# Performance work log

Measured on AMD Instinct MI355X. Metric: run time of the kernel, lower is better.

The kernel has to match this reference:

```python
import jax, jax.numpy as jnp
import numpy as np
from jax.ops import segment_sum

N_NODES = 50000
N_EDGES = 800000
NUM_FEAT = 16
EDGE_DIM = 8
H = 100
L = 2
BN_EPS = 1e-5


def setup_inputs() -> dict:
    key = jax.random.key(0)
    ks = iter(jax.random.split(key, 40))
    def w(shape, scale=0.05):
        return (jax.random.normal(next(ks), shape, dtype=jnp.float32) * scale)
    inp = {
        "x": jax.random.normal(next(ks), (N_NODES, NUM_FEAT), dtype=jnp.float32),
        "edge_index": jax.random.randint(next(ks), (2, N_EDGES), 0, N_NODES, dtype=jnp.int64) if jax.config.jax_enable_x64 else jax.random.randint(next(ks), (2, N_EDGES), 0, N_NODES).astype(jnp.int32),
        "edge_attr": jax.random.normal(next(ks), (N_EDGES, EDGE_DIM), dtype=jnp.float32),
        # embeddings
        "node_w": w((NUM_FEAT, H)), "node_b": w((H,)),
        "edge_w": w((EDGE_DIM, H)), "edge_b": w((H,)),
        # per-layer GINEConv MLP (stacked over layers)
        "conv_w1": w((L, H, H)), "conv_b1": w((L, H)),
        "conv_w2": w((L, H, H)), "conv_b2": w((L, H)),
        # batchnorm affine params
        "bn_gamma": jnp.ones((L, H), dtype=jnp.float32), "bn_beta": jnp.zeros((L, H), dtype=jnp.float32),
        # per-layer edge-update MLP
        "emlp_w1": w((L, 3 * H, H)), "emlp_b1": w((L, H)),
        "emlp_w2": w((L, H, H)), "emlp_b2": w((L, H)),
        # final classifier MLP (3H -> 50 -> 25 -> 2); dropout is identity at eval
        "mlp_w1": w((3 * H, 50)), "mlp_b1": w((50,)),
        "mlp_w2": w((50, 25)), "mlp_b2": w((25,)),
        "mlp_w3": w((25, 2)), "mlp_b3": w((2,)),
    }
    return inp


def reference(x, edge_index, edge_attr,
              node_w, node_b, edge_w, edge_b,
              conv_w1, conv_b1, conv_w2, conv_b2,
              bn_gamma, bn_beta,
              emlp_w1, emlp_b1, emlp_w2, emlp_b2,
              mlp_w1, mlp_b1, mlp_w2, mlp_b2, mlp_w3, mlp_b3):
    src, dst = edge_index[0], edge_index[1]
    n_nodes = x.shape[0]

    h = x @ node_w + node_b          # [N, H]
    e = edge_attr @ edge_w + edge_b  # [E, H]

    for i in range(L):
        # GINEConv: out_i = nn((1+eps)*h_i + sum_{e: dst=i} relu(h_src + e)); eps=0
        msg = jax.nn.relu(h[src] + e)                       # [E, H] gather + combine
        agg = segment_sum(msg, dst, num_segments=n_nodes)   # [N, H] scatter-add
        z = h + agg
        z = jax.nn.relu(z @ conv_w1[i] + conv_b1[i]) @ conv_w2[i] + conv_b2[i]
        # BatchNorm (train mode: batch stats over nodes, biased variance)
        mu = jnp.mean(z, axis=0)
        var = jnp.var(z, axis=0)
        z = (z - mu) * jax.lax.rsqrt(var + BN_EPS) * bn_gamma[i] + bn_beta[i]
        h = (h + jax.nn.relu(z)) * 0.5
        # edge update: e += MLP([h_src, h_dst, e]) / 2
        cat = jnp.concatenate([h[src], h[dst], e], axis=-1)  # [E, 3H]
        upd = jax.nn.relu(cat @ emlp_w1[i] + emlp_b1[i]) @ emlp_w2[i] + emlp_b2[i]
        e = e + upd * 0.5

    # per-edge features: relu([h_src, h_dst]) ++ e  -> [E, 3H]
    feat = jnp.concatenate([jax.nn.relu(jnp.concatenate([h[src], h[dst]], axis=-1)), e], axis=-1)
    out = jax.nn.relu(feat @ mlp_w1 + mlp_b1)
    out = jax.nn.relu(out @ mlp_w2 + mlp_b2)
    return out @ mlp_w3 + mlp_b3  # [E, 2]
```

## Files before the change

### kernel.cpp

```cpp
#include <hip/hip_runtime.h>
#include <hip/hip_bf16.h>

#define N_NODES 50000
#define N_EDGES 800000
#define HDIM 100
#define ESTR 104

typedef _Float16 half8_t __attribute__((ext_vector_type(8)));
typedef _Float16 half4_t __attribute__((ext_vector_type(4)));
typedef float f32x4_t __attribute__((ext_vector_type(4)));

struct FragDesc {
  const float* src; int stride; int K; int N; int outOff; int ksteps; int ntiles;
};
struct PrepArgs {
  FragDesc d[20];
  int prefix[21];
  int ndesc;
};

__global__ void k_prep_frags(PrepArgs args, _Float16* __restrict__ out) {
  int b = blockIdx.x;
  int di = 0;
  while (di + 1 < args.ndesc && b >= args.prefix[di + 1]) di++;
  FragDesc d = args.d[di];
  int local = b - args.prefix[di];
  int t = local / d.ksteps;
  int s = local % d.ksteps;
  int lane = threadIdx.x;
  int col = t * 16 + (lane & 15);
  int kb = s * 32 + (lane >> 4) * 8;
  _Float16* o = out + d.outOff + (size_t)((t * d.ksteps + s) * 64 + lane) * 8;
  #pragma unroll
  for (int i = 0; i < 8; ++i) {
    int k = kb + i;
    float v = (k < d.K && col < d.N) ? d.src[(size_t)k * d.stride + col] : 0.0f;
    o[i] = (_Float16)v;
  }
}

__global__ void k_ws_probe(float* out, float mb) { out[0] = mb; }

__global__ void k_hist(const int* __restrict__ dst, int* __restrict__ cnt) {
  for (int e = blockIdx.x * blockDim.x + threadIdx.x; e < N_EDGES;
       e += gridDim.x * blockDim.x)
    atomicAdd(&cnt[dst[e]], 1);
}

__global__ __launch_bounds__(1024) void k_scan(const int* __restrict__ cnt,
                                               int* __restrict__ rowptr,
                                               int* __restrict__ cursor) {
  __shared__ int part[1024];
  int t = threadIdx.x;
  const int CH = (N_NODES + 1023) / 1024;
  int base = t * CH;
  int s = 0;
  for (int i = 0; i < CH; ++i) {
    int n = base + i;
    if (n < N_NODES) s += cnt[n];
  }
  part[t] = s;
  __syncthreads();
  for (int off = 1; off < 1024; off <<= 1) {
    int v = 0;
    if (t >= off) v = part[t - off];
    __syncthreads();
    if (t >= off) part[t] += v;
    __syncthreads();
  }
  int run = (t == 0) ? 0 : part[t - 1];
  for (int i = 0; i < CH; ++i) {
    int n = base + i;
    if (n <= N_NODES) {
      rowptr[n] = run;
      if (n < N_NODES) { cursor[n] = run; run += cnt[n]; }
    }
  }
}

__global__ void k_perm(const int* __restrict__ src, const int* __restrict__ dst,
                       int* __restrict__ cursor, int* __restrict__ perm,
                       int* __restrict__ srcS) {
  for (int e = blockIdx.x * blockDim.x + threadIdx.x; e < N_EDGES;
       e += gridDim.x * blockDim.x) {
    int pos = atomicAdd(&cursor[dst[e]], 1);
    perm[pos] = e;
    srcS[pos] = src[e];
  }
}

template<bool L0>
__global__ __launch_bounds__(256) void k_agg(
    const int* __restrict__ rowptr, const int* __restrict__ perm,
    const int* __restrict__ srcS,
    const float* __restrict__ attr, const float* __restrict__ ew,
    const float* __restrict__ ebias,
    const _Float16* __restrict__ e,
    const float* __restrict__ h, float* __restrict__ agg) {
  __shared__ float EwL[800];
  __shared__ float ebL[128];
  int tid = threadIdx.x;
  if constexpr (L0) {
    for (int idx = tid; idx < 800; idx += 256) EwL[idx] = ew[idx];
    if (tid < 128) ebL[tid] = (tid < HDIM) ? ebias[tid] : 0.0f;
    __syncthreads();
  }
  int n = blockIdx.x * 2 + (tid >> 7);
  int j = tid & 127;
  if (n >= N_NODES || j >= HDIM) return;
  float acc = 0.0f;
  int p0 = rowptr[n], p1 = rowptr[n + 1];
  for (int pos = p0; pos < p1; ++pos) {
    int s = srcS[pos];
    int eid = perm[pos];
    float m;
    if constexpr (L0) {
      const float* ap = attr + (size_t)eid * 8;
      float e0 = ebL[j];
      #pragma unroll
      for (int k = 0; k < 8; ++k) e0 += ap[k] * EwL[k * HDIM + j];
      m = h[(size_t)s * HDIM + j] + e0;
    } else {
      m = h[(size_t)s * HDIM + j] + (float)e[(size_t)eid * ESTR + j];
    }
    acc += fmaxf(m, 0.0f);
  }
  agg[(size_t)n * HDIM + j] = acc;
}

__device__ __forceinline__ half8_t h8_zero() {
  half8_t a;
  #pragma unroll
  for (int i = 0; i < 8; ++i) a[i] = (_Float16)0.0f;
  return a;
}

__device__ __forceinline__ int swz_idx(int r, int c) {
  int chunk = (c >> 3) ^ (r & 7);
  return r * 128 + chunk * 8 + (c & 7);
}

template<int MODE>
__device__ __forceinline__ void load_a_node(const float* hp0,
                                            const float* ap0,
                                            int row, int lane, half8_t av[4]) {
  int g = lane >> 4;
  bool rv = (row < N_NODES);
  const float* hp = hp0 + (size_t)row * HDIM;
  const float* ap = ap0 + (size_t)row * HDIM;
  #pragma unroll
  for (int s = 0; s < 4; ++s) {
    int kb = s * 32 + g * 8;
    half8_t a = h8_zero();
    if (rv && kb < HDIM) {
      float f[8];
      #pragma unroll
      for (int i = 0; i < 8; ++i) f[i] = 0.0f;
      if (kb + 8 <= HDIM) {
        float4 v0 = *(const float4*)(hp + kb);
        float4 v1 = *(const float4*)(hp + kb + 4);
        f[0] = v0.x; f[1] = v0.y; f[2] = v0.z; f[3] = v0.w;
        f[4] = v1.x; f[5] = v1.y; f[6] = v1.z; f[7] = v1.w;
        if constexpr (MODE == 2) {
          float4 u0 = *(const float4*)(ap + kb);
          float4 u1 = *(const float4*)(ap + kb + 4);
          f[0] += u0.x; f[1] += u0.y; f[2] += u0.z; f[3] += u0.w;
          f[4] += u1.x; f[5] += u1.y; f[6] += u1.z; f[7] += u1.w;
        }
      } else {
        float4 v0 = *(const float4*)(hp + kb);
        f[0] = v0.x; f[1] = v0.y; f[2] = v0.z; f[3] = v0.w;
        if constexpr (MODE == 2) {
          float4 u0 = *(const float4*)(ap + kb);
          f[0] += u0.x; f[1] += u0.y; f[2] += u0.z; f[3] += u0.w;
        }
      }
      #pragma unroll
      for (int i = 0; i < 8; ++i) {
        float v = f[i];
        if constexpr (MODE == 1) v = fmaxf(v, 0.0f);
        a[i] = (_Float16)v;
      }
    }
    av[s] = a;
  }
}

template<int NT, int KS>
__device__ __forceinline__ void mfma_tiles(const half8_t* av, const _Float16* __restrict__ fb,
                                           int lane, f32x4_t* acc) {
  #pragma unroll
  for (int t = 0; t < NT; ++t) {
    #pragma unroll
    for (int s = 0; s < KS; ++s) {
      half8_t bv = *(const half8_t*)(fb + (size_t)(((t * KS + s) * 64 + lane) << 3));
      acc[t] = __builtin_amdgcn_mfma_f32_16x16x32_f16(av[s], bv, acc[t], 0, 0, 0);
    }
  }
}

template<int KS>
__device__ __forceinline__ void lds_read_a(const _Float16* L, int lane, half8_t* av) {
  int r = lane & 15;
  int g = lane >> 4;
  #pragma unroll
  for (int s = 0; s < KS; ++s) {
    int kb = s * 32 + g * 8;
    av[s] = *(const half8_t*)&L[swz_idx(r, kb)];
  }
}

__global__ void k_embed_h(const float* __restrict__ x, const float* __restrict__ w,
                          const float* __restrict__ bias, float* __restrict__ h) {
  int n = blockIdx.x;
  int j = threadIdx.x;
  if (j >= HDIM) return;
  float acc = bias[j];
  #pragma unroll
  for (int k = 0; k < 16; ++k) acc += x[n * 16 + k] * w[k * HDIM + j];
  h[(size_t)n * HDIM + j] = acc;
}

__global__ __launch_bounds__(256) void k_node_conv(
    const float* __restrict__ h, const float* agg,
    const _Float16* __restrict__ fb1, const _Float16* __restrict__ fb2,
    const float* __restrict__ b1, const float* __restrict__ b2,
    float* z, float* __restrict__ bn_sum, float* __restrict__ bn_sq) {
  __shared__ __align__(16) _Float16 lds[4][2048];
  int lane = threadIdx.x & 63;
  int wave = threadIdx.x >> 6;
  _Float16* L = lds[wave];
  int mbase = (blockIdx.x * 4 + wave) * 16;

  half8_t av[4];
  load_a_node<2>(h, agg, mbase + (lane & 15), lane, av);
  f32x4_t acc[7];
  #pragma unroll
  for (int t = 0; t < 7; ++t) acc[t] = (f32x4_t){0.f, 0.f, 0.f, 0.f};
  mfma_tiles<7, 4>(av, fb1, lane, acc);

  #pragma unroll
  for (int t = 0; t < 7; ++t) {
    int j = t * 16 + (lane & 15);
    float bias = (j < HDIM) ? b1[j] : 0.0f;
    #pragma unroll
    for (int q = 0; q < 4; ++q) {
      int r = (lane >> 4) * 4 + q;
      float v = fmaxf(acc[t][q] + bias, 0.0f);
      if (j >= HDIM) v = 0.0f;
      L[swz_idx(r, j)] = (_Float16)v;
    }
  }
  {
    int r = lane >> 2; int c0 = 112 + (lane & 3) * 4;
    #pragma unroll
    for (int i = 0; i < 4; ++i) L[swz_idx(r, c0 + i)] = (_Float16)0.0f;
  }
  __builtin_amdgcn_sched_barrier(0);

  half8_t av2[4];
  lds_read_a<4>(L, lane, av2);
  f32x4_t acc2[7];
  #pragma unroll
  for (int t = 0; t < 7; ++t) acc2[t] = (f32x4_t){0.f, 0.f, 0.f, 0.f};
  mfma_tiles<7, 4>(av2, fb2, lane, acc2);
  __builtin_amdgcn_sched_barrier(0);

  #pragma unroll
  for (int t = 0; t < 7; ++t) {
    int j = t * 16 + (lane & 15);
    float bias = (j < HDIM) ? b2[j] : 0.0f;
    float colsum = 0.0f, colsq = 0.0f;
    #pragma unroll
    for (int q = 0; q < 4; ++q) {
      int row = mbase + (lane >> 4) * 4 + q;
      float v = acc2[t][q] + bias;
      bool ok = (row < N_NODES) && (j < HDIM);
      if (ok) z[(size_t)row * HDIM + j] = v;
      float sv = ok ? v : 0.0f;
      colsum += sv; colsq += sv * sv;
    }
    colsum += __shfl_xor(colsum, 16);
    colsum += __shfl_xor(colsum, 32);
    colsq  += __shfl_xor(colsq, 16);
    colsq  += __shfl_xor(colsq, 32);
    if (lane < 16 && j < HDIM) {
      atomicAdd(&bn_sum[j], colsum);
      atomicAdd(&bn_sq[j], colsq);
    }
  }
}

__global__ void k_bn_final(const float* __restrict__ bn_sum, const float* __restrict__ bn_sq,
                           float* __restrict__ bn_mu, float* __restrict__ bn_rs) {
  int j = threadIdx.x;
  if (j >= HDIM) return;
  float mu = bn_sum[j] / (float)N_NODES;
  float var = bn_sq[j] / (float)N_NODES - mu * mu;
  bn_mu[j] = mu;
  bn_rs[j] = rsqrtf(var + 1e-5f);
}

__global__ void k_h_update(float* __restrict__ h, const float* __restrict__ z,
                           const float* __restrict__ bn_mu, const float* __restrict__ bn_rs,
                           const float* __restrict__ gamma, const float* __restrict__ beta) {
  int idx = blockIdx.x * blockDim.x + threadIdx.x;
  if (idx >= N_NODES * HDIM) return;
  int j = idx % HDIM;
  float zn = (z[idx] - bn_mu[j]) * bn_rs[j] * gamma[j] + beta[j];
  h[idx] = 0.5f * (h[idx] + fmaxf(zn, 0.0f));
}

template<bool RS>
__global__ __launch_bounds__(256) void k_node_gemm_t(const float* __restrict__ h,
                                                     const _Float16* __restrict__ fb,
                                                     _Float16* __restrict__ out) {
  constexpr int NT = RS ? 8 : 14;
  int lane = threadIdx.x & 63;
  int wave = threadIdx.x >> 6;
  int c = lane & 15;
  int mbase = (blockIdx.x * 4 + wave) * 16;
  half8_t av[4];
  load_a_node<RS ? 1 : 0>(h, h, mbase + c, lane, av);
  f32x4_t acc[NT];
  #pragma unroll
  for (int t = 0; t < NT; ++t) acc[t] = (f32x4_t){0.f, 0.f, 0.f, 0.f};
  mfma_tiles<NT, 4>(av, fb, lane, acc);
  #pragma unroll
  for (int q = 0; q < 4; ++q) {
    int row = mbase + (lane >> 4) * 4 + q;
    if (row >= N_NODES) continue;
    if constexpr (!RS) {
      half8_t hp, hq;
      #pragma unroll
      for (int t = 0; t < 8; ++t) {
        hp[t] = (t < 7) ? (_Float16)acc[t][q] : (_Float16)0.0f;
        hq[t] = (t < 7) ? (_Float16)acc[7 + t][q] : (_Float16)0.0f;
      }
      *(half8_t*)(out + (size_t)row * 256 + c * 8) = hp;
      *(half8_t*)(out + (size_t)row * 256 + 128 + c * 8) = hq;
    } else {
      half4_t hr, hs;
      #pragma unroll
      for (int t = 0; t < 4; ++t) {
        hr[t] = (_Float16)acc[t][q];
        hs[t] = (_Float16)acc[4 + t][q];
      }
      *(half4_t*)(out + (size_t)row * 128 + c * 4) = hr;
      *(half4_t*)(out + (size_t)row * 128 + 64 + c * 4) = hs;
    }
  }
}

__global__ __launch_bounds__(256) void k_edge0(
    const float* __restrict__ attr,
    const _Float16* __restrict__ PQ,
    const int* __restrict__ src, const int* __restrict__ dst,
    const float* __restrict__ ew, const float* __restrict__ ebias,
    const _Float16* __restrict__ fbW1c, const _Float16* __restrict__ fbW2,
    const float* __restrict__ b1, const float* __restrict__ b2,
    _Float16* __restrict__ e) {
  __shared__ __align__(16) _Float16 lds[4][2048];
  __shared__ float EwL[800];
  __shared__ float ebL[112];
  int tid = threadIdx.x;
  for (int idx = tid; idx < 800; idx += 256) EwL[idx] = ew[idx];
  if (tid < 112) ebL[tid] = (tid < HDIM) ? ebias[tid] : 0.0f;
  __syncthreads();

  int lane = tid & 63;
  int wave = tid >> 6;
  _Float16* L = lds[wave];
  int mbase = (blockIdx.x * 4 + wave) * 16;
  int c = lane & 15, g = lane >> 4;

  int sn[4], dn[4];
  #pragma unroll
  for (int q = 0; q < 4; ++q) {
    int row = mbase + g * 4 + q;
    sn[q] = src[row]; dn[q] = dst[row];
  }

  half8_t Pf[4], Qf[4];
  #pragma unroll
  for (int q = 0; q < 4; ++q) {
    Pf[q] = *(const half8_t*)(PQ + (size_t)sn[q] * 256 + c * 8);
    Qf[q] = *(const half8_t*)(PQ + (size_t)dn[q] * 256 + 128 + c * 8);
  }

  float af[4][8];
  #pragma unroll
  for (int q = 0; q < 4; ++q) {
    const float* ap = attr + (size_t)(mbase + g * 4 + q) * 8;
    float4 a0 = *(const float4*)ap;
    float4 a1 = *(const float4*)(ap + 4);
    af[q][0] = a0.x; af[q][1] = a0.y; af[q][2] = a0.z; af[q][3] = a0.w;
    af[q][4] = a1.x; af[q][5] = a1.y; af[q][6] = a1.z; af[q][7] = a1.w;
  }

  float e0r[7][4];
  #pragma unroll
  for (int t = 0; t < 7; ++t) {
    int j = t * 16 + c;
    #pragma unroll
    for (int q = 0; q < 4; ++q) {
      float v = 0.0f;
      if (j < HDIM) {
        v = ebL[j];
        #pragma unroll
        for (int k = 0; k < 8; ++k) v += af[q][k] * EwL[k * HDIM + j];
      }
      e0r[t][q] = v;
      L[swz_idx(g * 4 + q, j)] = (_Float16)v;
    }
  }
  { int r = lane >> 2; int c0 = 112 + (lane & 3) * 4;
    #pragma unroll
    for (int i = 0; i < 4; ++i) L[swz_idx(r, c0 + i)] = (_Float16)0.0f;
  }
  __builtin_amdgcn_sched_barrier(0);

  half8_t av[4];
  lds_read_a<4>(L, lane, av);
  __builtin_amdgcn_sched_barrier(0);
  f32x4_t acc[7];
  #pragma unroll
  for (int t = 0; t < 7; ++t) acc[t] = (f32x4_t){0.f, 0.f, 0.f, 0.f};
  mfma_tiles<7, 4>(av, fbW1c, lane, acc);

  #pragma unroll
  for (int t = 0; t < 7; ++t) {
    int j = t * 16 + c;
    float bias = (j < HDIM) ? b1[j] : 0.0f;
    #pragma unroll
    for (int q = 0; q < 4; ++q) {
      int r = g * 4 + q;
      float v = 0.0f;
      if (j < HDIM)
        v = fmaxf(acc[t][q] + bias + (float)Pf[q][t] + (float)Qf[q][t], 0.0f);
      L[swz_idx(r, j)] = (_Float16)v;
    }
  }
  __builtin_amdgcn_sched_barrier(0);

  half8_t av2[4];
  lds_read_a<4>(L, lane, av2);
  f32x4_t acc2[7];
  #pragma unroll
  for (int t = 0; t < 7; ++t) acc2[t] = (f32x4_t){0.f, 0.f, 0.f, 0.f};
  mfma_tiles<7, 4>(av2, fbW2, lane, acc2);
  __builtin_amdgcn_sched_barrier(0);

  #pragma unroll
  for (int t = 0; t < 7; ++t) {
    int j = t * 16 + c;
    float b2v = (j < HDIM) ? b2[j] : 0.0f;
    #pragma unroll
    for (int q = 0; q < 4; ++q) {
      int row = mbase + g * 4 + q;
      float eold = (float)(_Float16)e0r[t][q];
      float enew = eold + 0.5f * (acc2[t][q] + b2v);
      if (j < ESTR)
        e[(size_t)row * ESTR + j] = (j < HDIM) ? (_Float16)enew : (_Float16)0.0f;
    }
  }
}

__global__ __launch_bounds__(256) void k_edge1(
    const _Float16* __restrict__ e,
    const _Float16* __restrict__ PQ, const _Float16* __restrict__ RS,
    const int* __restrict__ src, const int* __restrict__ dst,
    const _Float16* __restrict__ fbW1c, const _Float16* __restrict__ fbW2,
    const float* __restrict__ b1, const float* __restrict__ b2,
    const _Float16* __restrict__ fbC, const _Float16* __restrict__ fbM2,
    const _Float16* __restrict__ fbM3,
    const float* __restrict__ mb1, const float* __restrict__ mb2,
    const float* __restrict__ mb3, float* __restrict__ out) {
  __shared__ __align__(16) _Float16 lds[4][2048];
  int lane = threadIdx.x & 63;
  int wave = threadIdx.x >> 6;
  _Float16* L = lds[wave];
  int mbase = (blockIdx.x * 4 + wave) * 16;
  int c = lane & 15, g = lane >> 4;

  int sn[4], dn[4];
  #pragma unroll
  for (int q = 0; q < 4; ++q) {
    int row = mbase + g * 4 + q;
    sn[q] = src[row]; dn[q] = dst[row];
  }

  half8_t Pf[4], Qf[4];
  #pragma unroll
  for (int q = 0; q < 4; ++q) {
    Pf[q] = *(const half8_t*)(PQ + (size_t)sn[q] * 256 + c * 8);
    Qf[q] = *(const half8_t*)(PQ + (size_t)dn[q] * 256 + 128 + c * 8);
  }

  half8_t av[4];
  {
    const _Float16* ep = e + (size_t)(mbase + c) * ESTR;
    #pragma unroll
    for (int s = 0; s < 3; ++s)
      av[s] = *(const half8_t*)(ep + s * 32 + g * 8);
    av[3] = (g == 0) ? *(const half8_t*)(ep + 96) : h8_zero();
  }
  #pragma unroll
  for (int s = 0; s < 4; ++s)
    *(half8_t*)&L[swz_idx(c, s * 32 + g * 8)] = av[s];
  __builtin_amdgcn_sched_barrier(0);
  _Float16 eoldv[7][4];
  #pragma unroll
  for (int t = 0; t < 7; ++t)
    #pragma unroll
    for (int q = 0; q < 4; ++q)
      eoldv[t][q] = L[swz_idx(g * 4 + q, t * 16 + c)];
  __builtin_amdgcn_sched_barrier(0);

  f32x4_t acc[7];
  #pragma unroll
  for (int t = 0; t < 7; ++t) acc[t] = (f32x4_t){0.f, 0.f, 0.f, 0.f};
  mfma_tiles<7, 4>(av, fbW1c, lane, acc);

  #pragma unroll
  for (int t = 0; t < 7; ++t) {
    int j = t * 16 + c;
    float bias = (j < HDIM) ? b1[j] : 0.0f;
    #pragma unroll
    for (int q = 0; q < 4; ++q) {
      int r = g * 4 + q;
      float v = 0.0f;
      if (j < HDIM)
        v = fmaxf(acc[t][q] + bias + (float)Pf[q][t] + (float)Qf[q][t], 0.0f);
      L[swz_idx(r, j)] = (_Float16)v;
    }
  }
  { int r = lane >> 2; int c0 = 112 + (lane & 3) * 4;
    #pragma unroll
    for (int i = 0; i < 4; ++i) L[swz_idx(r, c0 + i)] = (_Float16)0.0f;
  }
  __builtin_amdgcn_sched_barrier(0);

  half4_t Rf[4], Sf[4];
  #pragma unroll
  for (int q = 0; q < 4; ++q) {
    Rf[q] = *(const half4_t*)(RS + (size_t)sn[q] * 128 + c * 4);
    Sf[q] = *(const half4_t*)(RS + (size_t)dn[q] * 128 + 64 + c * 4);
  }

  half8_t av2[4];
  lds_read_a<4>(L, lane, av2);
  f32x4_t acc2[7];
  #pragma unroll
  for (int t = 0; t < 7; ++t) acc2[t] = (f32x4_t){0.f, 0.f, 0.f, 0.f};
  mfma_tiles<7, 4>(av2, fbW2, lane, acc2);
  __builtin_amdgcn_sched_barrier(0);

  #pragma unroll
  for (int t = 0; t < 7; ++t) {
    int j = t * 16 + c;
    float bias = (j < HDIM) ? b2[j] : 0.0f;
    #pragma unroll
    for (int q = 0; q < 4; ++q) {
      float v = 0.0f;
      if (j < HDIM)
        v = (float)eoldv[t][q] + 0.5f * (acc2[t][q] + bias);
      int r = g * 4 + q;
      L[swz_idx(r, j)] = (_Float16)v;
    }
  }
  __builtin_amdgcn_sched_barrier(0);

  half8_t av3[4];
  lds_read_a<4>(L, lane, av3);
  f32x4_t acc3[4];
  #pragma unroll
  for (int t = 0; t < 4; ++t) acc3[t] = (f32x4_t){0.f, 0.f, 0.f, 0.f};
  mfma_tiles<4, 4>(av3, fbC, lane, acc3);
  __builtin_amdgcn_sched_barrier(0);
  #pragma unroll
  for (int t = 0; t < 4; ++t) {
    int j = t * 16 + c;
    float bias = (j < 50) ? mb1[j] : 0.0f;
    #pragma unroll
    for (int q = 0; q < 4; ++q) {
      float v = 0.0f;
      if (j < 50)
        v = fmaxf(acc3[t][q] + bias + (float)Rf[q][t] + (float)Sf[q][t], 0.0f);
      int r = g * 4 + q;
      L[swz_idx(r, j)] = (_Float16)v;
    }
  }
  __builtin_amdgcn_sched_barrier(0);
  half8_t av4[2];
  lds_read_a<2>(L, lane, av4);
  f32x4_t acc4[2];
  #pragma unroll
  for (int t = 0; t < 2; ++t) acc4[t] = (f32x4_t){0.f, 0.f, 0.f, 0.f};
  mfma_tiles<2, 2>(av4, fbM2, lane, acc4);
  __builtin_amdgcn_sched_barrier(0);
  #pragma unroll
  for (int t = 0; t < 2; ++t) {
    int j = t * 16 + c;
    float bias = (j < 25) ? mb2[j] : 0.0f;
    #pragma unroll
    for (int q = 0; q < 4; ++q) {
      float v = (j < 25) ? fmaxf(acc4[t][q] + bias, 0.0f) : 0.0f;
      int r = g * 4 + q;
      L[swz_idx(r, j)] = (_Float16)v;
    }
  }
  __builtin_amdgcn_sched_barrier(0);
  half8_t av5[1];
  lds_read_a<1>(L, lane, av5);
  f32x4_t acc5 = (f32x4_t){0.f, 0.f, 0.f, 0.f};
  {
    half8_t bv = *(const half8_t*)(fbM3 + (size_t)(lane << 3));
    acc5 = __builtin_amdgcn_mfma_f32_16x16x32_f16(av5[0], bv, acc5, 0, 0, 0);
  }
  if (c < 2) {
    float bias = mb3[c];
    #pragma unroll
    for (int q = 0; q < 4; ++q) {
      int row = mbase + g * 4 + q;
      out[(size_t)row * 2 + c] = acc5[q] + bias;
    }
  }
}

extern "C" void kernel_launch(void* const* d_in, const int* in_sizes, int n_in,
                              void* d_out, int out_size, void* d_ws, size_t ws_size,
                              hipStream_t stream) {
  const float* x        = (const float*)d_in[0];
  const int*   ei       = (const int*)  d_in[1];
  const float* eattr    = (const float*)d_in[2];
  const float* node_w   = (const float*)d_in[3];
  const float* node_b   = (const float*)d_in[4];
  const float* edge_w   = (const float*)d_in[5];
  const float* edge_b   = (const float*)d_in[6];
  const float* conv_w1  = (const float*)d_in[7];
  const float* conv_b1  = (const float*)d_in[8];
  const float* conv_w2  = (const float*)d_in[9];
  const float* conv_b2  = (const float*)d_in[10];
  const float* bn_gamma = (const float*)d_in[11];
  const float* bn_beta  = (const float*)d_in[12];
  const float* emlp_w1  = (const float*)d_in[13];
  const float* emlp_b1  = (const float*)d_in[14];
  const float* emlp_w2  = (const float*)d_in[15];
  const float* emlp_b2  = (const float*)d_in[16];
  const float* mlp_w1   = (const float*)d_in[17];
  const float* mlp_b1   = (const float*)d_in[18];
  const float* mlp_w2   = (const float*)d_in[19];
  const float* mlp_b2   = (const float*)d_in[20];
  const float* mlp_w3   = (const float*)d_in[21];
  const float* mlp_b3   = (const float*)d_in[22];
  const int* src = ei;
  const int* dst = ei + N_EDGES;

  char* ws = (char*)d_ws;
  size_t off = 0;
  auto alloc = [&](size_t bytes) -> void* {
    void* p = ws + off;
    off += (bytes + 255) & ~(size_t)255;
    return p;
  };
  _Float16* e    = (_Float16*)alloc((size_t)N_EDGES * ESTR * 2);
  float* h       = (float*)alloc((size_t)N_NODES * HDIM * 4);
  float* agg     = (float*)alloc((size_t)N_NODES * HDIM * 4);
  _Float16* PQt  = (_Float16*)alloc((size_t)N_NODES * 256 * 2);
  int* cnt       = (int*)alloc((size_t)N_NODES * 4);
  int* cursor    = (int*)alloc((size_t)N_NODES * 4);
  int* rowptr    = (int*)alloc((size_t)(N_NODES + 1) * 4);
  int* perm      = (int*)alloc((size_t)N_EDGES * 4);
  int* srcS      = (int*)alloc((size_t)N_EDGES * 4);
  float* bn_sum  = (float*)alloc(512);
  float* bn_sq   = (float*)alloc(512);
  float* bn_mu   = (float*)alloc(512);
  float* bn_rs   = (float*)alloc(512);
  _Float16* frags = (_Float16*)alloc(200000 * 2);
  float* z = agg;
  _Float16* RSt = (_Float16*)agg;

  if (off > ws_size) {
    k_ws_probe<<<1, 1, 0, stream>>>((float*)d_out, (float)(ws_size >> 20));
    return;
  }

  PrepArgs pa;
  int nd = 0, tilesum = 0, fo = 0;
  auto add = [&](const float* sp, int stride, int K, int Ncols, int ksteps, int ntiles) -> int {
    pa.d[nd] = FragDesc{sp, stride, K, Ncols, fo, ksteps, ntiles};
    pa.prefix[nd] = tilesum;
    tilesum += ksteps * ntiles;
    ++nd;
    int ret = fo;
    fo += ksteps * ntiles * 512;
    return ret;
  };
  int offConvW1[2], offConvW2[2], offPQ[2], offW1c[2], offW2e[2];
  for (int i = 0; i < 2; ++i) {
    offConvW1[i] = add(conv_w1 + i * 10000, 100, 100, 100, 4, 7);
    offConvW2[i] = add(conv_w2 + i * 10000, 100, 100, 100, 4, 7);
    offPQ[i]     = add(emlp_w1 + i * 30000,         100, 100, 100, 4, 7);
                   add(emlp_w1 + i * 30000 + 10000, 100, 100, 100, 4, 7);
    offW1c[i]    = add(emlp_w1 + i * 30000 + 20000, 100, 100, 100, 4, 7);
    offW2e[i]    = add(emlp_w2 + i * 10000, 100, 100, 100, 4, 7);
  }
  int offRS = add(mlp_w1,         50, 100, 50, 4, 4);
              add(mlp_w1 + 5000,  50, 100, 50, 4, 4);
  int offC  = add(mlp_w1 + 10000, 50, 100, 50, 4, 4);
  int offM2 = add(mlp_w2, 25, 50, 25, 2, 2);
  int offM3 = add(mlp_w3, 2, 25, 2, 1, 1);
  pa.prefix[nd] = tilesum;
  pa.ndesc = nd;

  hipMemsetAsync(cnt, 0, (size_t)N_NODES * 4, stream);
  k_hist<<<2048, 256, 0, stream>>>(dst, cnt);
  k_scan<<<1, 1024, 0, stream>>>(cnt, rowptr, cursor);
  k_perm<<<2048, 256, 0, stream>>>(src, dst, cursor, perm, srcS);

  k_prep_frags<<<tilesum, 64, 0, stream>>>(pa, frags);
  k_embed_h<<<N_NODES, 128, 0, stream>>>(x, node_w, node_b, h);
  k_agg<true><<<N_NODES / 2, 256, 0, stream>>>(rowptr, perm, srcS,
                                               eattr, edge_w, edge_b,
                                               nullptr, h, agg);

  const int nodeGrid = (N_NODES + 63) / 64;
  for (int i = 0; i < 2; ++i) {
    hipMemsetAsync(bn_sum, 0, 512, stream);
    hipMemsetAsync(bn_sq, 0, 512, stream);
    k_node_conv<<<nodeGrid, 256, 0, stream>>>(h, agg, frags + offConvW1[i], frags + offConvW2[i],
                                              conv_b1 + i * 100, conv_b2 + i * 100,
                                              z, bn_sum, bn_sq);
    k_bn_final<<<1, 128, 0, stream>>>(bn_sum, bn_sq, bn_mu, bn_rs);
    k_h_update<<<(N_NODES * HDIM + 255) / 256, 256, 0, stream>>>(h, z, bn_mu, bn_rs,
                                                                 bn_gamma + i * 100, bn_beta + i * 100);
    k_node_gemm_t<false><<<nodeGrid, 256, 0, stream>>>(h, frags + offPQ[i], PQt);
    if (i == 0) {
      k_edge0<<<N_EDGES / 64, 256, 0, stream>>>(
          eattr, PQt, src, dst, edge_w, edge_b,
          frags + offW1c[0], frags + offW2e[0],
          emlp_b1, emlp_b2, e);
      k_agg<false><<<N_NODES / 2, 256, 0, stream>>>(rowptr, perm, srcS,
                                                    nullptr, nullptr, nullptr,
                                                    e, h, agg);
    } else {
      k_node_gemm_t<true><<<nodeGrid, 256, 0, stream>>>(h, frags + offRS, RSt);
      k_edge1<<<N_EDGES / 64, 256, 0, stream>>>(
          e, PQt, RSt, src, dst,
          frags + offW1c[1], frags + offW2e[1],
          emlp_b1 + 100, emlp_b2 + 100,
          frags + offC, frags + offM2, frags + offM3,
          mlp_b1, mlp_b2, mlp_b3, (float*)d_out);
    }
  }
}
```

Before: 1.596 ms.

## Process edges in dst-sorted order and fuse BN h-update into PQ GEMM

After: 1.505 ms (median of 2 runs). -5.7%, faster.

```diff
diff --git a/kernel.cpp b/kernel.cpp
--- a/kernel.cpp
+++ b/kernel.cpp
@@ -47,9 +47,9 @@
     atomicAdd(&cnt[dst[e]], 1);
 }
 
-__global__ __launch_bounds__(1024) void k_scan(const int* __restrict__ cnt,
-                                               int* __restrict__ rowptr,
-                                               int* __restrict__ cursor) {
+__global__ __launch_bounds__(1024) void k_scan(const int* cnt,
+                                               int* rowptr,
+                                               int* cursor) {
   __shared__ int part[1024];
   int t = threadIdx.x;
   const int CH = (N_NODES + 1023) / 1024;
@@ -73,19 +73,25 @@
     int n = base + i;
     if (n <= N_NODES) {
       rowptr[n] = run;
-      if (n < N_NODES) { cursor[n] = run; run += cnt[n]; }
+      if (n < N_NODES) {
+        int cv = cnt[n];
+        cursor[n] = run;
+        run += cv;
+      }
     }
   }
 }
 
 __global__ void k_perm(const int* __restrict__ src, const int* __restrict__ dst,
                        int* __restrict__ cursor, int* __restrict__ perm,
-                       int* __restrict__ srcS) {
+                       int* __restrict__ srcS, int* __restrict__ dstS) {
   for (int e = blockIdx.x * blockDim.x + threadIdx.x; e < N_EDGES;
        e += gridDim.x * blockDim.x) {
-    int pos = atomicAdd(&cursor[dst[e]], 1);
+    int d = dst[e];
+    int pos = atomicAdd(&cursor[d], 1);
     perm[pos] = e;
     srcS[pos] = src[e];
+    dstS[pos] = d;
   }
 }
 
@@ -112,16 +118,16 @@
   int p0 = rowptr[n], p1 = rowptr[n + 1];
   for (int pos = p0; pos < p1; ++pos) {
     int s = srcS[pos];
-    int eid = perm[pos];
     float m;
     if constexpr (L0) {
+      int eid = perm[pos];
       const float* ap = attr + (size_t)eid * 8;
       float e0 = ebL[j];
       #pragma unroll
       for (int k = 0; k < 8; ++k) e0 += ap[k] * EwL[k * HDIM + j];
       m = h[(size_t)s * HDIM + j] + e0;
     } else {
-      m = h[(size_t)s * HDIM + j] + (float)e[(size_t)eid * ESTR + j];
+      m = h[(size_t)s * HDIM + j] + (float)e[(size_t)pos * ESTR + j];
     }
     acc += fmaxf(m, 0.0f);
   }
@@ -251,8 +257,7 @@
       L[swz_idx(r, j)] = (_Float16)v;
     }
   }
-  {
-    int r = lane >> 2; int c0 = 112 + (lane & 3) * 4;
+  { int r = lane >> 2; int c0 = 112 + (lane & 3) * 4;
     #pragma unroll
     for (int i = 0; i < 4; ++i) L[swz_idx(r, c0 + i)] = (_Float16)0.0f;
   }
@@ -301,61 +306,126 @@
   bn_rs[j] = rsqrtf(var + 1e-5f);
 }
 
-__global__ void k_h_update(float* __restrict__ h, const float* __restrict__ z,
-                           const float* __restrict__ bn_mu, const float* __restrict__ bn_rs,
-                           const float* __restrict__ gamma, const float* __restrict__ beta) {
-  int idx = blockIdx.x * blockDim.x + threadIdx.x;
-  if (idx >= N_NODES * HDIM) return;
-  int j = idx % HDIM;
-  float zn = (z[idx] - bn_mu[j]) * bn_rs[j] * gamma[j] + beta[j];
-  h[idx] = 0.5f * (h[idx] + fmaxf(zn, 0.0f));
-}
-
-template<bool RS>
-__global__ __launch_bounds__(256) void k_node_gemm_t(const float* __restrict__ h,
-                                                     const _Float16* __restrict__ fb,
-                                                     _Float16* __restrict__ out) {
-  constexpr int NT = RS ? 8 : 14;
+__global__ __launch_bounds__(256) void k_h_pq(
+    float* h, const float* z,
+    const float* __restrict__ bn_mu, const float* __restrict__ bn_rs,
+    const float* __restrict__ gamma, const float* __restrict__ beta,
+    const _Float16* __restrict__ fb, _Float16* __restrict__ PQt) {
+  int lane = threadIdx.x & 63;
+  int wave = threadIdx.x >> 6;
+  int c = lane & 15, g = lane >> 4;
+  int mbase = (blockIdx.x * 4 + wave) * 16;
+  int row = mbase + c;
+  bool rv = row < N_NODES;
+  float* hp = h + (size_t)row * HDIM;
+  const float* zp = z + (size_t)row * HDIM;
+
+  half8_t av[4];
+  #pragma unroll
+  for (int s = 0; s < 4; ++s) {
+    int kb = s * 32 + g * 8;
+    half8_t a = h8_zero();
+    if (rv && kb < HDIM) {
+      int lim = (kb + 8 <= HDIM) ? 8 : 4;
+      float zf[8], hf[8], mu[8], rs[8], ga[8], be[8];
+      { float4 v = *(const float4*)(zp + kb);
+        zf[0]=v.x; zf[1]=v.y; zf[2]=v.z; zf[3]=v.w; }
+      { float4 v = *(const float4*)(hp + kb);
+        hf[0]=v.x; hf[1]=v.y; hf[2]=v.z; hf[3]=v.w; }
+      { float4 v = *(const float4*)(bn_mu + kb);
+        mu[0]=v.x; mu[1]=v.y; mu[2]=v.z; mu[3]=v.w; }
+      { float4 v = *(const float4*)(bn_rs + kb);
+        rs[0]=v.x; rs[1]=v.y; rs[2]=v.z; rs[3]=v.w; }
+      { float4 v = *(const float4*)(gamma + kb);
+        ga[0]=v.x; ga[1]=v.y; ga[2]=v.z; ga[3]=v.w; }
+      { float4 v = *(const float4*)(beta + kb);
+        be[0]=v.x; be[1]=v.y; be[2]=v.z; be[3]=v.w; }
+      if (lim == 8) {
+        { float4 v = *(const float4*)(zp + kb + 4);
+          zf[4]=v.x; zf[5]=v.y; zf[6]=v.z; zf[7]=v.w; }
+        { float4 v = *(const float4*)(hp + kb + 4);
+          hf[4]=v.x; hf[5]=v.y; hf[6]=v.z; hf[7]=v.w; }
+        { float4 v = *(const float4*)(bn_mu + kb + 4);
+          mu[4]=v.x; mu[5]=v.y; mu[6]=v.z; mu[7]=v.w; }
+        { float4 v = *(const float4*)(bn_rs + kb + 4);
+          rs[4]=v.x; rs[5]=v.y; rs[6]=v.z; rs[7]=v.w; }
+        { float4 v = *(const float4*)(gamma + kb + 4);
+          ga[4]=v.x; ga[5]=v.y; ga[6]=v.z; ga[7]=v.w; }
+        { float4 v = *(const float4*)(beta + kb + 4);
+          be[4]=v.x; be[5]=v.y; be[6]=v.z; be[7]=v.w; }
+      }
+      float hn[8];
+      #pragma unroll
+      for (int i = 0; i < 8; ++i) hn[i] = 0.0f;
+      for (int i = 0; i < 8; ++i) {
+        if (i < lim) {
+          float zn = (zf[i] - mu[i]) * rs[i] * ga[i] + be[i];
+          hn[i] = 0.5f * (hf[i] + fmaxf(zn, 0.0f));
+          a[i] = (_Float16)hn[i];
+        }
+      }
+      { float4 v; v.x=hn[0]; v.y=hn[1]; v.z=hn[2]; v.w=hn[3];
+        *(float4*)(hp + kb) = v; }
+      if (lim == 8) {
+        float4 v; v.x=hn[4]; v.y=hn[5]; v.z=hn[6]; v.w=hn[7];
+        *(float4*)(hp + kb + 4) = v;
+      }
+    }
+    av[s] = a;
+  }
+
+  f32x4_t acc[14];
+  #pragma unroll
+  for (int t = 0; t < 14; ++t) acc[t] = (f32x4_t){0.f, 0.f, 0.f, 0.f};
+  mfma_tiles<14, 4>(av, fb, lane, acc);
+  #pragma unroll
+  for (int q = 0; q < 4; ++q) {
+    int orow = mbase + (lane >> 4) * 4 + q;
+    if (orow >= N_NODES) continue;
+    half8_t hp8, hq8;
+    #pragma unroll
+    for (int t = 0; t < 8; ++t) {
+      hp8[t] = (t < 7) ? (_Float16)acc[t][q] : (_Float16)0.0f;
+      hq8[t] = (t < 7) ? (_Float16)acc[7 + t][q] : (_Float16)0.0f;
+    }
+    *(half8_t*)(PQt + (size_t)orow * 256 + c * 8) = hp8;
+    *(half8_t*)(PQt + (size_t)orow * 256 + 128 + c * 8) = hq8;
+  }
+}
+
+__global__ __launch_bounds__(256) void k_node_rs(const float* __restrict__ h,
+                                                 const _Float16* __restrict__ fb,
+                                                 _Float16* __restrict__ out) {
   int lane = threadIdx.x & 63;
   int wave = threadIdx.x >> 6;
   int c = lane & 15;
   int mbase = (blockIdx.x * 4 + wave) * 16;
   half8_t av[4];
-  load_a_node<RS ? 1 : 0>(h, h, mbase + c, lane, av);
-  f32x4_t acc[NT];
-  #pragma unroll
-  for (int t = 0; t < NT; ++t) acc[t] = (f32x4_t){0.f, 0.f, 0.f, 0.f};
-  mfma_tiles<NT, 4>(av, fb, lane, acc);
+  load_a_node<1>(h, h, mbase + c, lane, av);
+  f32x4_t acc[8];
+  #pragma unroll
+  for (int t = 0; t < 8; ++t) acc[t] = (f32x4_t){0.f, 0.f, 0.f, 0.f};
+  mfma_tiles<8, 4>(av, fb, lane, acc);
   #pragma unroll
   for (int q = 0; q < 4; ++q) {
     int row = mbase + (lane >> 4) * 4 + q;
     if (row >= N_NODES) continue;
-    if constexpr (!RS) {
-      half8_t hp, hq;
-      #pragma unroll
-      for (int t = 0; t < 8; ++t) {
-        hp[t] = (t < 7) ? (_Float16)acc[t][q] : (_Float16)0.0f;
-        hq[t] = (t < 7) ? (_Float16)acc[7 + t][q] : (_Float16)0.0f;
-      }
-      *(half8_t*)(out + (size_t)row * 256 + c * 8) = hp;
-      *(half8_t*)(out + (size_t)row * 256 + 128 + c * 8) = hq;
-    } else {
-      half4_t hr, hs;
-      #pragma unroll
-      for (int t = 0; t < 4; ++t) {
-        hr[t] = (_Float16)acc[t][q];
-        hs[t] = (_Float16)acc[4 + t][q];
-      }
-      *(half4_t*)(out + (size_t)row * 128 + c * 4) = hr;
-      *(half4_t*)(out + (size_t)row * 128 + 64 + c * 4) = hs;
-    }
+    half4_t hr, hs;
+    #pragma unroll
+    for (int t = 0; t < 4; ++t) {
+      hr[t] = (_Float16)acc[t][q];
+      hs[t] = (_Float16)acc[4 + t][q];
+    }
+    *(half4_t*)(out + (size_t)row * 128 + c * 4) = hr;
+    *(half4_t*)(out + (size_t)row * 128 + 64 + c * 4) = hs;
   }
 }
 
 __global__ __launch_bounds__(256) void k_edge0(
     const float* __restrict__ attr,
     const _Float16* __restrict__ PQ,
-    const int* __restrict__ src, const int* __restrict__ dst,
+    const int* __restrict__ srcS, const int* __restrict__ dstS,
+    const int* __restrict__ perm,
     const float* __restrict__ ew, const float* __restrict__ ebias,
     const _Float16* __restrict__ fbW1c, const _Float16* __restrict__ fbW2,
     const float* __restrict__ b1, const float* __restrict__ b2,
@@ -374,11 +444,11 @@
   int mbase = (blockIdx.x * 4 + wave) * 16;
   int c = lane & 15, g = lane >> 4;
 
-  int sn[4], dn[4];
+  int sn[4], dn[4], pv[4];
   #pragma unroll
   for (int q = 0; q < 4; ++q) {
     int row = mbase + g * 4 + q;
-    sn[q] = src[row]; dn[q] = dst[row];
+    sn[q] = srcS[row]; dn[q] = dstS[row]; pv[q] = perm[row];
   }
 
   half8_t Pf[4], Qf[4];
@@ -391,7 +461,7 @@
   float af[4][8];
   #pragma unroll
   for (int q = 0; q < 4; ++q) {
-    const float* ap = attr + (size_t)(mbase + g * 4 + q) * 8;
+    const float* ap = attr + (size_t)pv[q] * 8;
     float4 a0 = *(const float4*)ap;
     float4 a1 = *(const float4*)(ap + 4);
     af[q][0] = a0.x; af[q][1] = a0.y; af[q][2] = a0.z; af[q][3] = a0.w;
@@ -469,7 +539,8 @@
 __global__ __launch_bounds__(256) void k_edge1(
     const _Float16* __restrict__ e,
     const _Float16* __restrict__ PQ, const _Float16* __restrict__ RS,
-    const int* __restrict__ src, const int* __restrict__ dst,
+    const int* __restrict__ srcS, const int* __restrict__ dstS,
+    const int* __restrict__ perm,
     const _Float16* __restrict__ fbW1c, const _Float16* __restrict__ fbW2,
     const float* __restrict__ b1, const float* __restrict__ b2,
     const _Float16* __restrict__ fbC, const _Float16* __restrict__ fbM2,
@@ -483,39 +554,27 @@
   int mbase = (blockIdx.x * 4 + wave) * 16;
   int c = lane & 15, g = lane >> 4;
 
+  half8_t av[4];
+  {
+    const _Float16* ep = e + (size_t)(mbase + c) * ESTR;
+    #pragma unroll
+    for (int s = 0; s < 3; ++s)
+      av[s] = *(const half8_t*)(ep + s * 32 + g * 8);
+    av[3] = (g == 0) ? *(const half8_t*)(ep + 96) : h8_zero();
+  }
+
   int sn[4], dn[4];
   #pragma unroll
   for (int q = 0; q < 4; ++q) {
     int row = mbase + g * 4 + q;
-    sn[q] = src[row]; dn[q] = dst[row];
-  }
-
+    sn[q] = srcS[row]; dn[q] = dstS[row];
+  }
   half8_t Pf[4], Qf[4];
   #pragma unroll
   for (int q = 0; q < 4; ++q) {
     Pf[q] = *(const half8_t*)(PQ + (size_t)sn[q] * 256 + c * 8);
     Qf[q] = *(const half8_t*)(PQ + (size_t)dn[q] * 256 + 128 + c * 8);
   }
-
-  half8_t av[4];
-  {
-    const _Float16* ep = e + (size_t)(mbase + c) * ESTR;
-    #pragma unroll
-    for (int s = 0; s < 3; ++s)
-      av[s] = *(const half8_t*)(ep + s * 32 + g * 8);
-    av[3] = (g == 0) ? *(const half8_t*)(ep + 96) : h8_zero();
-  }
-  #pragma unroll
-  for (int s = 0; s < 4; ++s)
-    *(half8_t*)&L[swz_idx(c, s * 32 + g * 8)] = av[s];
-  __builtin_amdgcn_sched_barrier(0);
-  _Float16 eoldv[7][4];
-  #pragma unroll
-  for (int t = 0; t < 7; ++t)
-    #pragma unroll
-    for (int q = 0; q < 4; ++q)
-      eoldv[t][q] = L[swz_idx(g * 4 + q, t * 16 + c)];
-  __builtin_amdgcn_sched_barrier(0);
 
   f32x4_t acc[7];
   #pragma unroll
@@ -562,9 +621,12 @@
     float bias = (j < HDIM) ? b2[j] : 0.0f;
     #pragma unroll
     for (int q = 0; q < 4; ++q) {
+      int row = mbase + g * 4 + q;
       float v = 0.0f;
-      if (j < HDIM)
-        v = (float)eoldv[t][q] + 0.5f * (acc2[t][q] + bias);
+      if (j < HDIM) {
+        float eold = (float)e[(size_t)row * ESTR + j];
+        v = eold + 0.5f * (acc2[t][q] + bias);
+      }
       int r = g * 4 + q;
       L[swz_idx(r, j)] = (_Float16)v;
     }
@@ -623,7 +685,7 @@
     #pragma unroll
     for (int q = 0; q < 4; ++q) {
       int row = mbase + g * 4 + q;
-      out[(size_t)row * 2 + c] = acc5[q] + bias;
+      out[(size_t)perm[row] * 2 + c] = acc5[q] + bias;
     }
   }
 }
@@ -668,11 +730,11 @@
   float* h       = (float*)alloc((size_t)N_NODES * HDIM * 4);
   float* agg     = (float*)alloc((size_t)N_NODES * HDIM * 4);
   _Float16* PQt  = (_Float16*)alloc((size_t)N_NODES * 256 * 2);
-  int* cnt       = (int*)alloc((size_t)N_NODES * 4);
   int* cursor    = (int*)alloc((size_t)N_NODES * 4);
   int* rowptr    = (int*)alloc((size_t)(N_NODES + 1) * 4);
   int* perm      = (int*)alloc((size_t)N_EDGES * 4);
   int* srcS      = (int*)alloc((size_t)N_EDGES * 4);
+  int* dstS      = (int*)alloc((size_t)N_EDGES * 4);
   float* bn_sum  = (float*)alloc(512);
   float* bn_sq   = (float*)alloc(512);
   float* bn_mu   = (float*)alloc(512);
@@ -714,10 +776,10 @@
   pa.prefix[nd] = tilesum;
   pa.ndesc = nd;
 
-  hipMemsetAsync(cnt, 0, (size_t)N_NODES * 4, stream);
-  k_hist<<<2048, 256, 0, stream>>>(dst, cnt);
-  k_scan<<<1, 1024, 0, stream>>>(cnt, rowptr, cursor);
-  k_perm<<<2048, 256, 0, stream>>>(src, dst, cursor, perm, srcS);
+  hipMemsetAsync(cursor, 0, (size_t)N_NODES * 4, stream);
+  k_hist<<<2048, 256, 0, stream>>>(dst, cursor);
+  k_scan<<<1, 1024, 0, stream>>>(cursor, rowptr, cursor);
+  k_perm<<<2048, 256, 0, stream>>>(src, dst, cursor, perm, srcS, dstS);
 
   k_prep_frags<<<tilesum, 64, 0, stream>>>(pa, frags);
   k_embed_h<<<N_NODES, 128, 0, stream>>>(x, node_w, node_b, h);
@@ -733,21 +795,21 @@
                                               conv_b1 + i * 100, conv_b2 + i * 100,
                                               z, bn_sum, bn_sq);
     k_bn_final<<<1, 128, 0, stream>>>(bn_sum, bn_sq, bn_mu, bn_rs);
-    k_h_update<<<(N_NODES * HDIM + 255) / 256, 256, 0, stream>>>(h, z, bn_mu, bn_rs,
-                                                                 bn_gamma + i * 100, bn_beta + i * 100);
-    k_node_gemm_t<false><<<nodeGrid, 256, 0, stream>>>(h, frags + offPQ[i], PQt);
+    k_h_pq<<<nodeGrid, 256, 0, stream>>>(h, z, bn_mu, bn_rs,
+                                         bn_gamma + i * 100, bn_beta + i * 100,
+                                         frags + offPQ[i], PQt);
     if (i == 0) {
       k_edge0<<<N_EDGES / 64, 256, 0, stream>>>(
-          eattr, PQt, src, dst, edge_w, edge_b,
+          eattr, PQt, srcS, dstS, perm, edge_w, edge_b,
           frags + offW1c[0], frags + offW2e[0],
           emlp_b1, emlp_b2, e);
       k_agg<false><<<N_NODES / 2, 256, 0, stream>>>(rowptr, perm, srcS,
                                                     nullptr, nullptr, nullptr,
                                                     e, h, agg);
     } else {
-      k_node_gemm_t<true><<<nodeGrid, 256, 0, stream>>>(h, frags + offRS, RSt);
+      k_node_rs<<<nodeGrid, 256, 0, stream>>>(h, frags + offRS, RSt);
       k_edge1<<<N_EDGES / 64, 256, 0, stream>>>(
-          e, PQt, RSt, src, dst,
+          e, PQt, RSt, srcS, dstS, perm,
           frags + offW1c[1], frags + offW2e[1],
           emlp_b1 + 100, emlp_b2 + 100,
           frags + offC, frags + offM2, frags + offM3,
```
